# Kernel tuning notes

Measured on AMD Instinct MI355X. Metric: run time of the kernel, lower is better.

The kernel has to match this reference:

```python
import jax, jax.numpy as jnp
import numpy as np

Q, N, C, H, W = 200, 25, 640, 5, 5
TEMPERATURE = 0.1
EPS = 1e-8  # torch F.cosine_similarity eps


def setup_inputs() -> dict:
    key = jax.random.key(0)
    k1, k2 = jax.random.split(key)
    feature_q = jax.random.normal(k1, (Q, N, C, H, W), dtype=jnp.float32)
    feature_s = jax.random.normal(k2, (Q, N, C, H, W), dtype=jnp.float32)
    return {"feature_q": feature_q, "feature_s": feature_s}


def reference(feature_q, feature_s):
    # Correlation volume: contract over channels c -> [Q, N, Hs, Ws, Hq, Wq]
    corr = jnp.einsum('qncij,qnckl->qnijkl', feature_s, feature_q)

    # Co-attention: mean-pool over the opposite spatial dims, softmax over last axis
    s_att = jax.nn.softmax(corr.mean(axis=(4, 5)), axis=-1)  # [Q, N, Hs, Ws]
    q_att = jax.nn.softmax(corr.mean(axis=(2, 3)), axis=-1)  # [Q, N, Hq, Wq]

    # Support aggregation (mode='support'):
    # torch broadcast [1,Q,N,1,H,W]*[1,Q,N,C,H,W] then mean(dim=1)
    # == mean over q of s_att[q,n,h,w] * feature_s[q,n,c,h,w] -> [1,N,C,H,W]
    attended_s = (s_att[:, :, None, :, :] * feature_s).mean(axis=0, keepdims=True)

    # Query aggregation (mode='query'):
    # torch broadcast [1,Q',N,1,H,W]*[Q,1,N,C,H,W] then mean(dim=1=Q')
    # == feature_q[q,n,c,h,w] * mean_{q'} q_att[q',n,h,w] -> [Q,N,C,H,W]
    # (fused form: avoids materializing the [Q,Q,N,C,H,W] intermediate)
    attended_q = feature_q * q_att.mean(axis=0)[None, :, None, :, :]

    # Cosine similarity along last dim (W), torch semantics with eps clamp
    dot = jnp.sum(attended_s * attended_q, axis=-1)               # [Q,N,C,H]
    norm_s = jnp.maximum(jnp.sqrt(jnp.sum(attended_s * attended_s, axis=-1)), EPS)
    norm_q = jnp.maximum(jnp.sqrt(jnp.sum(attended_q * attended_q, axis=-1)), EPS)
    similarity_score = dot / (norm_s * norm_q) / TEMPERATURE      # [Q,N,C,H]
    return similarity_score
```

## Files before the change

kernel.cpp:

```cpp
#include <hip/hip_runtime.h>

constexpr int Qn = 200;
constexpr int Nn = 25;
constexpr int Cn = 640;
constexpr int Hn = 5;
constexpr int Wn = 5;
constexpr int HWn = Hn * Wn;
constexpr int CHW = Cn * HWn;
constexpr float TEMP_INV = 10.0f;
constexpr float EPSC = 1e-8f;

__global__ __launch_bounds__(256) void attn_kernel(
    const float* __restrict__ fq, const float* __restrict__ fs,
    float* __restrict__ s_att, float* __restrict__ qbar)
{
    __shared__ float buf[6400];
    __shared__ float sums[256];

    const int qn   = blockIdx.x;
    const int n    = qn % Nn;
    const int tid  = threadIdx.x;
    const int lane = tid & 63;
    const int wave = tid >> 6;

    const float4* fq4 = (const float4*)(fq + (size_t)qn * CHW);
    const float4* fs4 = (const float4*)(fs + (size_t)qn * CHW);

    const bool is_s = (tid >= 128);
    const int rbase = is_s ? 3200 + (tid - 128) * HWn : tid * HWn;

    float acc[HWn];
#pragma unroll
    for (int p = 0; p < HWn; ++p) acc[p] = 0.f;

    for (int t = 0; t < 5; ++t) {
        __syncthreads();
        const int off = t * 800;
#pragma unroll
        for (int k = 0; k < 6; ++k) {
            const int j = tid + k * 256;
            const float4 v = (j < 800) ? fq4[off + j] : fs4[off + j - 800];
            *(float4*)&buf[j * 4] = v;
        }
        if (tid < 64) {
            const int j = tid + 1536;
            *(float4*)&buf[j * 4] = fs4[off + j - 800];
        }
        __syncthreads();

        const float* row = &buf[rbase];
        float r[HWn];
        float s = 0.f;
#pragma unroll
        for (int p = 0; p < HWn; ++p) { r[p] = row[p]; s += r[p]; }
        sums[tid] = s;
        __syncthreads();

        const float ps = is_s ? sums[tid - 128] : sums[tid + 128];
#pragma unroll
        for (int p = 0; p < HWn; ++p) acc[p] += r[p] * ps;
    }

    __syncthreads();

#pragma unroll
    for (int p = 0; p < HWn; ++p) {
        float a = acc[p];
#pragma unroll
        for (int d = 1; d < 64; d <<= 1) a += __shfl_xor(a, d);
        acc[p] = a;
    }
    if (lane == 0) {
#pragma unroll
        for (int p = 0; p < HWn; ++p) sums[wave * HWn + p] = acc[p];
    }
    __syncthreads();
    if (tid < 50) {
        float v;
        if (tid < 25) v = sums[50 + tid] + sums[75 + tid];
        else          v = sums[tid - 25] + sums[tid];
        sums[100 + tid] = v;
    }
    __syncthreads();

    if (tid < 10) {
        const float* fm = &sums[100];
        const int r = tid;
        const float* row = (r < 5) ? &fm[r * 5] : &fm[HWn + (r - 5) * 5];
        float v[5];
        float mx = -1e30f;
#pragma unroll
        for (int j = 0; j < 5; ++j) {
            v[j] = row[j] * (1.0f / HWn);
            mx = fmaxf(mx, v[j]);
        }
        float s = 0.f;
#pragma unroll
        for (int j = 0; j < 5; ++j) { v[j] = __expf(v[j] - mx); s += v[j]; }
        const float inv = 1.0f / s;
        if (r < 5) {
#pragma unroll
            for (int j = 0; j < 5; ++j)
                s_att[(size_t)qn * HWn + r * 5 + j] = v[j] * inv;
        } else {
#pragma unroll
            for (int j = 0; j < 5; ++j)
                atomicAdd(&qbar[n * HWn + (r - 5) * 5 + j],
                          v[j] * inv * (1.0f / Qn));
        }
    }
}

__global__ __launch_bounds__(256) void agg_kernel(
    const float* __restrict__ fs, const float* __restrict__ s_att,
    float* __restrict__ att_s)
{
    constexpr int QCH = 40;
    __shared__ float w_lds[QCH * HWn];
    const int n  = blockIdx.y;
    const int q0 = blockIdx.z * QCH;

    for (int i = threadIdx.x; i < QCH * HWn; i += 256) {
        const int q = q0 + i / HWn;
        const int hw = i % HWn;
        w_lds[i] = s_att[(size_t)(q * Nn + n) * HWn + hw];
    }
    __syncthreads();

    const int f4 = blockIdx.x * 256 + threadIdx.x;
    if (f4 >= CHW / 4) return;
    const int f = f4 * 4;
    const int hw0 = f % HWn, hw1 = (f + 1) % HWn,
              hw2 = (f + 2) % HWn, hw3 = (f + 3) % HWn;

    float4 acc = make_float4(0.f, 0.f, 0.f, 0.f);
#pragma unroll 4
    for (int qi = 0; qi < QCH; ++qi) {
        const int q = q0 + qi;
        const float4 v = *(const float4*)(fs + (size_t)(q * Nn + n) * CHW + f);
        const float* w = &w_lds[qi * HWn];
        acc.x += w[hw0] * v.x;
        acc.y += w[hw1] * v.y;
        acc.z += w[hw2] * v.z;
        acc.w += w[hw3] * v.w;
    }
    float* dst = att_s + (size_t)n * CHW + f;
    atomicAdd(dst + 0, acc.x * (1.0f / Qn));
    atomicAdd(dst + 1, acc.y * (1.0f / Qn));
    atomicAdd(dst + 2, acc.z * (1.0f / Qn));
    atomicAdd(dst + 3, acc.w * (1.0f / Qn));
}

__global__ __launch_bounds__(256) void cos_kernel(
    const float* __restrict__ fq, const float* __restrict__ att_s,
    const float* __restrict__ qbar, float* __restrict__ out)
{
    const size_t idx = (size_t)blockIdx.x * 256 + threadIdx.x;
    if (idx >= (size_t)Qn * Nn * Cn * Hn) return;
    const int h = (int)(idx % Hn);
    const size_t t = idx / Hn;
    const int c = (int)(t % Cn);
    const size_t qn = t / Cn;
    const int n = (int)(qn % Nn);

    const float* fqr = fq + (qn * Cn + c) * HWn + h * Wn;
    const float* asr = att_s + ((size_t)n * Cn + c) * HWn + h * Wn;
    const float* qb  = qbar + n * HWn + h * Wn;

    float dot = 0.f, ns2 = 0.f, nq2 = 0.f;
#pragma unroll
    for (int w = 0; w < Wn; ++w) {
        const float aq = fqr[w] * qb[w];
        const float as = asr[w];
        dot += as * aq;
        ns2 += as * as;
        nq2 += aq * aq;
    }
    const float ns = fmaxf(sqrtf(ns2), EPSC);
    const float nq = fmaxf(sqrtf(nq2), EPSC);
    out[idx] = dot / (ns * nq) * TEMP_INV;
}

extern "C" void kernel_launch(void* const* d_in, const int* in_sizes, int n_in,
                              void* d_out, int out_size, void* d_ws, size_t ws_size,
                              hipStream_t stream)
{
    const float* fq = (const float*)d_in[0];
    const float* fs = (const float*)d_in[1];
    float* out = (float*)d_out;

    float* s_att = (float*)d_ws;
    float* qbar  = s_att + (size_t)Qn * Nn * HWn;
    float* att_s = qbar + 1024;

    hipMemsetAsync(qbar, 0, (1024 + (size_t)Nn * CHW) * sizeof(float), stream);

    attn_kernel<<<Qn * Nn, 256, 0, stream>>>(fq, fs, s_att, qbar);

    dim3 g2((CHW / 4 + 255) / 256, Nn, 5);
    agg_kernel<<<g2, 256, 0, stream>>>(fs, s_att, att_s);

    const size_t total = (size_t)Qn * Nn * Cn * Hn;
    cos_kernel<<<(unsigned)((total + 255) / 256), 256, 0, stream>>>(fq, att_s, qbar, out);
}
```

Measured before the change: 757.7 us.

## Drop Q-split atomics in support aggregation; one block covers all Q

The support aggregation kernel now loops over all 200 queries per thread in 64-thread blocks rather than splitting Q into five chunks. Each thread writes its float4 result directly, so the atomicAdds and the memset of the att_s buffer go away. The cost is fewer, smaller blocks (250 instead of 125x... roughly 250 per n, 6250 total) with longer serial loops and a bigger per-block LDS weight load of 5000 floats by only 64 threads, which may reduce latency hiding.

```diff
diff --git a/kernel.cpp b/kernel.cpp
--- a/kernel.cpp
+++ b/kernel.cpp
@@ -111,44 +111,39 @@
     }
 }
 
-__global__ __launch_bounds__(256) void agg_kernel(
+__global__ __launch_bounds__(64) void agg_kernel(
     const float* __restrict__ fs, const float* __restrict__ s_att,
     float* __restrict__ att_s)
 {
-    constexpr int QCH = 40;
-    __shared__ float w_lds[QCH * HWn];
-    const int n  = blockIdx.y;
-    const int q0 = blockIdx.z * QCH;
-
-    for (int i = threadIdx.x; i < QCH * HWn; i += 256) {
-        const int q = q0 + i / HWn;
+    __shared__ float w_lds[Qn * HWn];
+    const int n = blockIdx.y;
+
+    for (int i = threadIdx.x; i < Qn * HWn; i += 64) {
+        const int q = i / HWn;
         const int hw = i % HWn;
         w_lds[i] = s_att[(size_t)(q * Nn + n) * HWn + hw];
     }
     __syncthreads();
 
-    const int f4 = blockIdx.x * 256 + threadIdx.x;
-    if (f4 >= CHW / 4) return;
-    const int f = f4 * 4;
+    const int j = blockIdx.x * 64 + threadIdx.x;
+    if (j >= CHW / 4) return;
+    const int f = j * 4;
     const int hw0 = f % HWn, hw1 = (f + 1) % HWn,
               hw2 = (f + 2) % HWn, hw3 = (f + 3) % HWn;
 
     float4 acc = make_float4(0.f, 0.f, 0.f, 0.f);
-#pragma unroll 4
-    for (int qi = 0; qi < QCH; ++qi) {
-        const int q = q0 + qi;
+#pragma unroll 8
+    for (int q = 0; q < Qn; ++q) {
         const float4 v = *(const float4*)(fs + (size_t)(q * Nn + n) * CHW + f);
-        const float* w = &w_lds[qi * HWn];
+        const float* w = &w_lds[q * HWn];
         acc.x += w[hw0] * v.x;
         acc.y += w[hw1] * v.y;
         acc.z += w[hw2] * v.z;
         acc.w += w[hw3] * v.w;
     }
-    float* dst = att_s + (size_t)n * CHW + f;
-    atomicAdd(dst + 0, acc.x * (1.0f / Qn));
-    atomicAdd(dst + 1, acc.y * (1.0f / Qn));
-    atomicAdd(dst + 2, acc.z * (1.0f / Qn));
-    atomicAdd(dst + 3, acc.w * (1.0f / Qn));
+    float4* dst = (float4*)(att_s + (size_t)n * CHW + f);
+    *dst = make_float4(acc.x * (1.0f / Qn), acc.y * (1.0f / Qn),
+                       acc.z * (1.0f / Qn), acc.w * (1.0f / Qn));
 }
 
 __global__ __launch_bounds__(256) void cos_kernel(
@@ -193,12 +188,12 @@
     float* qbar  = s_att + (size_t)Qn * Nn * HWn;
     float* att_s = qbar + 1024;
 
-    hipMemsetAsync(qbar, 0, (1024 + (size_t)Nn * CHW) * sizeof(float), stream);
+    hipMemsetAsync(qbar, 0, 1024 * sizeof(float), stream);
 
     attn_kernel<<<Qn * Nn, 256, 0, stream>>>(fq, fs, s_att, qbar);
 
-    dim3 g2((CHW / 4 + 255) / 256, Nn, 5);
-    agg_kernel<<<g2, 256, 0, stream>>>(fs, s_att, att_s);
+    dim3 g2((CHW / 4 + 63) / 64, Nn);
+    agg_kernel<<<g2, 64, 0, stream>>>(fs, s_att, att_s);
 
     const size_t total = (size_t)Qn * Nn * Cn * Hn;
     cos_kernel<<<(unsigned)((total + 255) / 256), 256, 0, stream>>>(fq, att_s, qbar, out);
```

After: 752.8 us. Within noise of the previous version (-0.6%).
